# Kernel optimization log

Measured on AMD Instinct MI355X. Metric: run time of the kernel, lower is better.

The kernel has to match this reference:

```python
import jax, jax.numpy as jnp
import numpy as np

D_MODEL = 2048
NUM_HEADS = 32
NUM_GROUPS = 8
D_K = D_MODEL // NUM_HEADS          # 64
HPG = NUM_HEADS // NUM_GROUPS       # heads per group = 4
B, S = 2, 2048


def setup_inputs() -> dict:
    key = jax.random.key(0)
    ks = jax.random.split(key, 9)
    w_scale = 0.02
    kv_dim = NUM_GROUPS * D_K
    return {
        "x":  jax.random.normal(ks[0], (B, S, D_MODEL), dtype=jnp.float32),
        "Wq": jax.random.normal(ks[1], (D_MODEL, D_MODEL), dtype=jnp.float32) * w_scale,
        "bq": jnp.zeros((D_MODEL,), dtype=jnp.float32),
        "Wk": jax.random.normal(ks[2], (D_MODEL, kv_dim), dtype=jnp.float32) * w_scale,
        "bk": jnp.zeros((kv_dim,), dtype=jnp.float32),
        "Wv": jax.random.normal(ks[3], (D_MODEL, kv_dim), dtype=jnp.float32) * w_scale,
        "bv": jnp.zeros((kv_dim,), dtype=jnp.float32),
        "Wo": jax.random.normal(ks[4], (D_MODEL, D_MODEL), dtype=jnp.float32) * w_scale,
        "bo": jnp.zeros((D_MODEL,), dtype=jnp.float32),
    }


def reference(x, Wq, bq, Wk, bk, Wv, bv, Wo, bo):
    b, s, _ = x.shape
    # projections (torch Linear math: x @ W^T + b, here weights stored as (in,out))
    Q = (x @ Wq + bq).reshape(b, s, NUM_HEADS, D_K).transpose(0, 2, 1, 3)   # [B,H,S,dk]
    Kg = (x @ Wk + bk).reshape(b, s, NUM_GROUPS, D_K).transpose(0, 2, 1, 3)  # [B,G,S,dk]
    Vg = (x @ Wv + bv).reshape(b, s, NUM_GROUPS, D_K).transpose(0, 2, 1, 3)
    # repeat_interleave K/V over head dim to full head count
    K = jnp.repeat(Kg, HPG, axis=1)  # [B,H,S,dk]
    V = jnp.repeat(Vg, HPG, axis=1)
    scores = jnp.einsum("bhqd,bhkd->bhqk", Q, K) / np.sqrt(D_K).astype(np.float32)
    attn = jax.nn.softmax(scores, axis=-1)
    out = jnp.einsum("bhqk,bhkd->bhqd", attn, V)               # [B,H,S,dk]
    out = out.transpose(0, 2, 1, 3).reshape(b, s, D_MODEL)
    out = out @ Wo + bo
    # module returns grouped K,V cache: K[:, ::HPG] == Kg
    return out, (Kg, Vg)
```

## Files before the change

### kernel.cpp

```cpp
#include <hip/hip_runtime.h>
#include <hip/hip_bf16.h>
#include <stdint.h>

#define S_LEN 2048
#define DM    2048
#define NH    32
#define NG    8
#define DK    64
#define BATCH 2
#define MROWS (BATCH*S_LEN)
#define NQKV  3072
#define SSCALE 0.18033688f

typedef __bf16 bf16x8 __attribute__((ext_vector_type(8)));
typedef short  s16x8  __attribute__((ext_vector_type(8)));
typedef float  f32x4  __attribute__((ext_vector_type(4)));
typedef unsigned int u32x4 __attribute__((ext_vector_type(4)));

__device__ __forceinline__ unsigned short f2b(float f) {
    unsigned int x = __float_as_uint(f);
    unsigned int r = (x + 0x7fffu + ((x >> 16) & 1u)) >> 16;
    return (unsigned short)r;
}
__device__ __forceinline__ bf16x8 ld8(const unsigned short* p) {
    return *(const bf16x8*)p;
}
__device__ __forceinline__ s16x8 cvt8(const float* p) {
    f32x4 a = *(const f32x4*)p;
    f32x4 b = *(const f32x4*)(p + 4);
    s16x8 o;
#pragma unroll
    for (int j = 0; j < 4; j++) { o[j] = (short)f2b(a[j]); o[4 + j] = (short)f2b(b[j]); }
    return o;
}
__device__ __forceinline__ void gl_lds(const unsigned short* g, unsigned short* l) {
    __builtin_amdgcn_global_load_lds(
        (const __attribute__((address_space(1))) unsigned int*)g,
        (__attribute__((address_space(3))) unsigned int*)l, 16, 0, 0);
}
__device__ __forceinline__ void wait_dma() {
    asm volatile("s_waitcnt vmcnt(0)" ::: "memory");
}

__global__ __launch_bounds__(256) void cvt_x(const float* __restrict__ in,
                                             unsigned short* __restrict__ out) {
    size_t id = (size_t)blockIdx.x * 256 + threadIdx.x;
    *(s16x8*)&out[id * 8] = cvt8(in + id * 8);
}

__global__ void transpose_cvt(const float* __restrict__ in,
                              unsigned short* __restrict__ out, int R, int C) {
    __shared__ float t[32][33];
    int c0 = blockIdx.x * 32, r0 = blockIdx.y * 32;
    int tx = threadIdx.x, ty = threadIdx.y;
#pragma unroll
    for (int i = 0; i < 4; i++)
        t[ty + i * 8][tx] = in[(size_t)(r0 + ty + i * 8) * C + c0 + tx];
    __syncthreads();
#pragma unroll
    for (int i = 0; i < 4; i++)
        out[(size_t)(c0 + ty + i * 8) * R + r0 + tx] = f2b(t[tx][ty + i * 8]);
}

__global__ void bias_concat(const float* __restrict__ bq, const float* __restrict__ bk,
                            const float* __restrict__ bv, float* __restrict__ o) {
    int i = blockIdx.x * 256 + threadIdx.x;
    if (i < 2048) o[i] = bq[i];
    else if (i < 2560) o[i] = bk[i - 2048];
    else if (i < 3072) o[i] = bv[i - 2560];
}

__global__ __launch_bounds__(256) void gemm_qkv(const unsigned short* __restrict__ A,
                                                const unsigned short* __restrict__ Bt,
                                                const float* __restrict__ bias,
                                                unsigned short* __restrict__ Qb,
                                                float* __restrict__ Kg, float* __restrict__ Vg,
                                                unsigned short* __restrict__ Kb,
                                                unsigned short* __restrict__ Vtb) {
    __shared__ alignas(16) unsigned short As[128 * 32];
    __shared__ alignas(16) unsigned short Bs[128 * 32];
    const int K = DM;
    const int tid = threadIdx.x;
    const int n0 = blockIdx.x * 128, m0 = blockIdx.y * 128;
    const int w = tid >> 6, lane = tid & 63;
    const int ln15 = lane & 15, quad = lane >> 4;
    const int wm = (w >> 1) * 64, wn = (w & 1) * 64;
    const int xq = (quad ^ (ln15 & 3)) * 8;
    f32x4 acc[4][4] = {};
    for (int k0 = 0; k0 < K; k0 += 32) {
        __syncthreads();
#pragma unroll
        for (int i = 0; i < 2; ++i) {
            int s = w * 128 + i * 64 + lane;
            int r = s >> 2, cb = (s & 3) ^ (r & 3);
            gl_lds(&A[(size_t)(m0 + r) * K + k0 + cb * 8], &As[(w * 128 + i * 64) * 8]);
            gl_lds(&Bt[(size_t)(n0 + r) * K + k0 + cb * 8], &Bs[(w * 128 + i * 64) * 8]);
        }
        wait_dma();
        __syncthreads();
        bf16x8 af[4], bfr[4];
#pragma unroll
        for (int mt = 0; mt < 4; mt++)
            af[mt] = ld8(&As[(wm + mt * 16 + ln15) * 32 + xq]);
#pragma unroll
        for (int nt = 0; nt < 4; nt++)
            bfr[nt] = ld8(&Bs[(wn + nt * 16 + ln15) * 32 + xq]);
#pragma unroll
        for (int mt = 0; mt < 4; mt++)
#pragma unroll
            for (int nt = 0; nt < 4; nt++)
                acc[mt][nt] = __builtin_amdgcn_mfma_f32_16x16x32_bf16(af[mt], bfr[nt], acc[mt][nt], 0, 0, 0);
    }
#pragma unroll
    for (int nt = 0; nt < 4; nt++) {
        int col = n0 + wn + nt * 16 + ln15;
        float bv = bias[col];
#pragma unroll
        for (int mt = 0; mt < 4; mt++) {
            int row0 = m0 + wm + mt * 16 + quad * 4;
#pragma unroll
            for (int r = 0; r < 4; r++) {
                float val = acc[mt][nt][r] + bv;
                int row = row0 + r;
                int b = row >> 11, s = row & 2047;
                if (col < 2048) {
                    Qb[(size_t)row * DM + col] = f2b(val * SSCALE);
                } else if (col < 2560) {
                    int gc = col - 2048, g = gc >> 6, d = gc & 63;
                    size_t idx = (((size_t)(b * NG + g) * S_LEN + s) << 6) + d;
                    Kg[idx] = val;
                    Kb[idx] = f2b(val);
                } else {
                    int gc = col - 2560, g = gc >> 6, d = gc & 63;
                    Vg[(((size_t)(b * NG + g) * S_LEN + s) << 6) + d] = val;
                    Vtb[((size_t)(b * NG + g) * DK + d) * S_LEN + s] = f2b(val);
                }
            }
        }
    }
}

__global__ __launch_bounds__(256) void gemm_o(const unsigned short* __restrict__ A,
                                              const unsigned short* __restrict__ Bt,
                                              const float* __restrict__ bias,
                                              float* __restrict__ C) {
    __shared__ alignas(16) unsigned short As[128 * 32];
    __shared__ alignas(16) unsigned short Bs[128 * 32];
    const int K = DM, N = DM;
    const int tid = threadIdx.x;
    const int n0 = blockIdx.x * 128, m0 = blockIdx.y * 128;
    const int w = tid >> 6, lane = tid & 63;
    const int ln15 = lane & 15, quad = lane >> 4;
    const int wm = (w >> 1) * 64, wn = (w & 1) * 64;
    const int xq = (quad ^ (ln15 & 3)) * 8;
    f32x4 acc[4][4] = {};
    for (int k0 = 0; k0 < K; k0 += 32) {
        __syncthreads();
#pragma unroll
        for (int i = 0; i < 2; ++i) {
            int s = w * 128 + i * 64 + lane;
            int r = s >> 2, cb = (s & 3) ^ (r & 3);
            gl_lds(&A[(size_t)(m0 + r) * K + k0 + cb * 8], &As[(w * 128 + i * 64) * 8]);
            gl_lds(&Bt[(size_t)(n0 + r) * K + k0 + cb * 8], &Bs[(w * 128 + i * 64) * 8]);
        }
        wait_dma();
        __syncthreads();
        bf16x8 af[4], bfr[4];
#pragma unroll
        for (int mt = 0; mt < 4; mt++)
            af[mt] = ld8(&As[(wm + mt * 16 + ln15) * 32 + xq]);
#pragma unroll
        for (int nt = 0; nt < 4; nt++)
            bfr[nt] = ld8(&Bs[(wn + nt * 16 + ln15) * 32 + xq]);
#pragma unroll
        for (int mt = 0; mt < 4; mt++)
#pragma unroll
            for (int nt = 0; nt < 4; nt++)
                acc[mt][nt] = __builtin_amdgcn_mfma_f32_16x16x32_bf16(af[mt], bfr[nt], acc[mt][nt], 0, 0, 0);
    }
#pragma unroll
    for (int nt = 0; nt < 4; nt++) {
        int col = n0 + wn + nt * 16 + ln15;
        float bv = bias[col];
#pragma unroll
        for (int mt = 0; mt < 4; mt++) {
            int row0 = m0 + wm + mt * 16 + quad * 4;
#pragma unroll
            for (int r = 0; r < 4; r++)
                C[(size_t)(row0 + r) * N + col] = acc[mt][nt][r] + bv;
        }
    }
}

#define MT 2
__global__ __launch_bounds__(256, 4) void attn_fwd(const unsigned short* __restrict__ Qb,
                                                   const unsigned short* __restrict__ Kb,
                                                   const unsigned short* __restrict__ Vtb,
                                                   unsigned short* __restrict__ AO) {
    __shared__ alignas(16) unsigned short Ks[2][64 * 64];
    __shared__ alignas(16) unsigned short Vt[2][64 * 64];
    const int b = blockIdx.z, h = blockIdx.y, q0 = blockIdx.x * (MT * 64);
    const int g = h >> 2;
    const int tid = threadIdx.x;
    const int w = tid >> 6, lane = tid & 63;
    const int ln15 = lane & 15, quad = lane >> 4;
    const int x7a = (quad ^ (ln15 & 7)) * 8;
    const int x7b = x7a ^ 32;

    bf16x8 aq[MT][2];
#pragma unroll
    for (int mt = 0; mt < MT; mt++) {
        const size_t qrow =
            ((size_t)(b * S_LEN + q0 + w * (MT * 16) + mt * 16 + ln15)) * DM + h * DK;
        aq[mt][0] = ld8(&Qb[qrow + quad * 8]);
        aq[mt][1] = ld8(&Qb[qrow + 32 + quad * 8]);
    }

    bf16x8 ones;
#pragma unroll
    for (int j = 0; j < 8; j++) ones[j] = (__bf16)1.0f;

    f32x4 o[MT][4] = {};
    f32x4 l_acc[MT] = {};
    const size_t kvb = ((size_t)(b * NG + g)) * S_LEN * DK;

#define STAGE(k0v, buf) do {                                                     \
    _Pragma("unroll")                                                            \
    for (int i = 0; i < 2; i++) {                                                \
        int s = w * 128 + i * 64 + lane;                                         \
        int r = s >> 3, cb = (s & 7) ^ (r & 7);                                  \
        gl_lds(&Kb[kvb + (size_t)((k0v) + r) * DK + cb * 8],                     \
               &Ks[buf][(w * 128 + i * 64) * 8]);                                \
        gl_lds(&Vtb[kvb + (size_t)r * S_LEN + (k0v) + cb * 8],                   \
               &Vt[buf][(w * 128 + i * 64) * 8]);                                \
    } } while (0)

    STAGE(0, 0);
    wait_dma();
    __syncthreads();
    int cur = 0;

    for (int k0 = 0; k0 < S_LEN; k0 += 64) {
        if (k0 + 64 < S_LEN) STAGE(k0 + 64, cur ^ 1);

        f32x4 z[MT][4];
        __builtin_amdgcn_s_setprio(1);
#pragma unroll
        for (int nt = 0; nt < 4; nt++) {
            bf16x8 bk0 = ld8(&Ks[cur][(nt * 16 + ln15) * 64 + x7a]);
            bf16x8 bk1 = ld8(&Ks[cur][(nt * 16 + ln15) * 64 + x7b]);
#pragma unroll
            for (int mt = 0; mt < MT; mt++) {
                f32x4 t = {0.f, 0.f, 0.f, 0.f};
                t = __builtin_amdgcn_mfma_f32_16x16x32_bf16(bk0, aq[mt][0], t, 0, 0, 0);
                t = __builtin_amdgcn_mfma_f32_16x16x32_bf16(bk1, aq[mt][1], t, 0, 0, 0);
                z[mt][nt] = t;
            }
        }
        __builtin_amdgcn_s_setprio(0);

        bf16x8 pa[MT][2];
#pragma unroll
        for (int mt = 0; mt < MT; mt++) {
            unsigned int S[4][2];
#pragma unroll
            for (int nt = 0; nt < 4; nt++) {
                f32x4 pe;
#pragma unroll
                for (int r = 0; r < 4; r++)
                    pe[r] = __builtin_amdgcn_exp2f(z[mt][nt][r]);
                asm("v_cvt_pk_bf16_f32 %0, %1, %2" : "=v"(S[nt][0]) : "v"(pe[0]), "v"(pe[1]));
                asm("v_cvt_pk_bf16_f32 %0, %1, %2" : "=v"(S[nt][1]) : "v"(pe[2]), "v"(pe[3]));
            }
#pragma unroll
            for (int f = 0; f < 2; f++) {
                unsigned int wA[2], wB[2];
#pragma unroll
                for (int p = 0; p < 2; p++) {
                    unsigned int xa = S[2 * f][p], yb = S[2 * f + 1][p];
                    asm("v_permlane32_swap_b32 %0, %1" : "+v"(xa), "+v"(yb));
                    asm("v_permlane16_swap_b32 %0, %1" : "+v"(xa), "+v"(yb));
                    wA[p] = xa; wB[p] = yb;
                }
                u32x4 t4;
                t4[0] = wA[0]; t4[1] = wA[1]; t4[2] = wB[0]; t4[3] = wB[1];
                pa[mt][f] = __builtin_bit_cast(bf16x8, t4);
            }
        }

        __builtin_amdgcn_s_setprio(1);
#pragma unroll
        for (int nt = 0; nt < 4; nt++) {
            bf16x8 bv0 = ld8(&Vt[cur][(nt * 16 + ln15) * 64 + x7a]);
            bf16x8 bv1 = ld8(&Vt[cur][(nt * 16 + ln15) * 64 + x7b]);
#pragma unroll
            for (int mt = 0; mt < MT; mt++) {
                f32x4 t = o[mt][nt];
                t = __builtin_amdgcn_mfma_f32_16x16x32_bf16(pa[mt][0], bv0, t, 0, 0, 0);
                t = __builtin_amdgcn_mfma_f32_16x16x32_bf16(pa[mt][1], bv1, t, 0, 0, 0);
                o[mt][nt] = t;
            }
        }
#pragma unroll
        for (int mt = 0; mt < MT; mt++) {
            l_acc[mt] = __builtin_amdgcn_mfma_f32_16x16x32_bf16(pa[mt][0], ones, l_acc[mt], 0, 0, 0);
            l_acc[mt] = __builtin_amdgcn_mfma_f32_16x16x32_bf16(pa[mt][1], ones, l_acc[mt], 0, 0, 0);
        }
        __builtin_amdgcn_s_setprio(0);

        wait_dma();
        __syncthreads();
        cur ^= 1;
    }
#undef STAGE

#pragma unroll
    for (int mt = 0; mt < MT; mt++) {
#pragma unroll
        for (int r = 0; r < 4; r++) {
            float inv = 1.0f / l_acc[mt][r];
            int q = q0 + w * (MT * 16) + mt * 16 + quad * 4 + r;
#pragma unroll
            for (int nt = 0; nt < 4; nt++) {
                int col = h * DK + nt * 16 + ln15;
                *(__bf16*)&AO[((size_t)(b * S_LEN + q)) * DM + col] =
                    (__bf16)(o[mt][nt][r] * inv);
            }
        }
    }
}

extern "C" void kernel_launch(void* const* d_in, const int* in_sizes, int n_in,
                              void* d_out, int out_size, void* d_ws, size_t ws_size,
                              hipStream_t stream) {
    const float* x  = (const float*)d_in[0];
    const float* Wq = (const float*)d_in[1];
    const float* bq = (const float*)d_in[2];
    const float* Wk = (const float*)d_in[3];
    const float* bk = (const float*)d_in[4];
    const float* Wv = (const float*)d_in[5];
    const float* bv = (const float*)d_in[6];
    const float* Wo = (const float*)d_in[7];
    const float* bo = (const float*)d_in[8];

    float* out = (float*)d_out;
    float* Kg  = out + (size_t)MROWS * DM;
    float* Vg  = Kg + (size_t)BATCH * NG * S_LEN * DK;

    unsigned short* Qb = (unsigned short*)d_out;

    unsigned short* ws    = (unsigned short*)d_ws;
    unsigned short* WqkvT = ws;
    unsigned short* WoT   = WqkvT + (size_t)NQKV * DM;
    unsigned short* Kb    = WoT + (size_t)DM * DM;
    unsigned short* Vtb   = Kb + (size_t)BATCH * NG * S_LEN * DK;
    unsigned short* AO    = Vtb + (size_t)BATCH * NG * S_LEN * DK;
    unsigned short* xb    = AO + (size_t)MROWS * DM;
    float*          bqkv  = (float*)(xb + (size_t)MROWS * DM);

    hipLaunchKernelGGL(cvt_x, dim3(MROWS * DM / 8 / 256), dim3(256), 0, stream, x, xb);

    dim3 tb(32, 8);
    hipLaunchKernelGGL(transpose_cvt, dim3(DM / 32, DM / 32), tb, 0, stream,
                       Wq, WqkvT, DM, DM);
    hipLaunchKernelGGL(transpose_cvt, dim3(512 / 32, DM / 32), tb, 0, stream,
                       Wk, WqkvT + (size_t)2048 * DM, DM, 512);
    hipLaunchKernelGGL(transpose_cvt, dim3(512 / 32, DM / 32), tb, 0, stream,
                       Wv, WqkvT + (size_t)2560 * DM, DM, 512);
    hipLaunchKernelGGL(transpose_cvt, dim3(DM / 32, DM / 32), tb, 0, stream,
                       Wo, WoT, DM, DM);
    hipLaunchKernelGGL(bias_concat, dim3(12), dim3(256), 0, stream, bq, bk, bv, bqkv);

    hipLaunchKernelGGL(gemm_qkv, dim3(NQKV / 128, MROWS / 128), dim3(256), 0, stream,
                       xb, WqkvT, bqkv, Qb, Kg, Vg, Kb, Vtb);

    hipLaunchKernelGGL(attn_fwd, dim3(S_LEN / (MT * 64), NH, BATCH), dim3(256), 0, stream,
                       Qb, Kb, Vtb, AO);

    hipLaunchKernelGGL(gemm_o, dim3(DM / 128, MROWS / 128), dim3(256), 0, stream,
                       AO, WoT, bo, out);
}
```

Before: 360.2 us.

## Double-buffer LDS in QKV and output GEMMs with new swizzle and MFMA priority

Both projection GEMMs now keep two LDS stages, so the global-to-LDS DMA for the next K tile is issued before the current tile's MFMAs. This removes one barrier per iteration and overlaps load latency with compute. The LDS XOR swizzle changes from (row&3) to ((row>>1)&3) to cut bank conflicts. The MFMA block is wrapped in s_setprio and launch bounds now request 4 blocks per CU. The cost is doubled LDS use per block (32KB) and more register pressure.

```diff
diff --git a/kernel.cpp b/kernel.cpp
--- a/kernel.cpp
+++ b/kernel.cpp
@@ -70,47 +70,60 @@
     else if (i < 3072) o[i] = bv[i - 2560];
 }
 
-__global__ __launch_bounds__(256) void gemm_qkv(const unsigned short* __restrict__ A,
+__global__ __launch_bounds__(256, 4) void gemm_qkv(const unsigned short* __restrict__ A,
                                                 const unsigned short* __restrict__ Bt,
                                                 const float* __restrict__ bias,
                                                 unsigned short* __restrict__ Qb,
                                                 float* __restrict__ Kg, float* __restrict__ Vg,
                                                 unsigned short* __restrict__ Kb,
                                                 unsigned short* __restrict__ Vtb) {
-    __shared__ alignas(16) unsigned short As[128 * 32];
-    __shared__ alignas(16) unsigned short Bs[128 * 32];
+    __shared__ alignas(16) unsigned short As[2][128 * 32];
+    __shared__ alignas(16) unsigned short Bs[2][128 * 32];
     const int K = DM;
     const int tid = threadIdx.x;
     const int n0 = blockIdx.x * 128, m0 = blockIdx.y * 128;
     const int w = tid >> 6, lane = tid & 63;
     const int ln15 = lane & 15, quad = lane >> 4;
     const int wm = (w >> 1) * 64, wn = (w & 1) * 64;
-    const int xq = (quad ^ (ln15 & 3)) * 8;
+    const int xq = (quad ^ ((ln15 >> 1) & 3)) * 8;
     f32x4 acc[4][4] = {};
+
+#define GSTAGE(k0v, buf) do {                                                    \
+    _Pragma("unroll")                                                            \
+    for (int i = 0; i < 2; ++i) {                                                \
+        int s = w * 128 + i * 64 + lane;             \
+        int r = s >> 2, cb = (s & 3) ^ ((r >> 1) & 3);                           \
+        gl_lds(&A[(size_t)(m0 + r) * K + (k0v) + cb * 8],                        \
+               &As[buf][(w * 128 + i * 64) * 8]);                                \
+        gl_lds(&Bt[(size_t)(n0 + r) * K + (k0v) + cb * 8],                       \
+               &Bs[buf][(w * 128 + i * 64) * 8]);                                \
+    } } while (0)
+
+    GSTAGE(0, 0);
+    wait_dma();
+    __syncthreads();
+    int cur = 0;
     for (int k0 = 0; k0 < K; k0 += 32) {
-        __syncthreads();
-#pragma unroll
-        for (int i = 0; i < 2; ++i) {
-            int s = w * 128 + i * 64 + lane;
-            int r = s >> 2, cb = (s & 3) ^ (r & 3);
-            gl_lds(&A[(size_t)(m0 + r) * K + k0 + cb * 8], &As[(w * 128 + i * 64) * 8]);
-            gl_lds(&Bt[(size_t)(n0 + r) * K + k0 + cb * 8], &Bs[(w * 128 + i * 64) * 8]);
-        }
+        if (k0 + 32 < K) GSTAGE(k0 + 32, cur ^ 1);
+        bf16x8 af[4], bfr[4];
+#pragma unroll
+        for (int mt = 0; mt < 4; mt++)
+            af[mt] = ld8(&As[cur][(wm + mt * 16 + ln15) * 32 + xq]);
+#pragma unroll
+        for (int nt = 0; nt < 4; nt++)
+            bfr[nt] = ld8(&Bs[cur][(wn + nt * 16 + ln15) * 32 + xq]);
+        __builtin_amdgcn_s_setprio(1);
+#pragma unroll
+        for (int mt = 0; mt < 4; mt++)
+#pragma unroll
+            for (int nt = 0; nt < 4; nt++)
+                acc[mt][nt] = __builtin_amdgcn_mfma_f32_16x16x32_bf16(af[mt], bfr[nt], acc[mt][nt], 0, 0, 0);
+        __builtin_amdgcn_s_setprio(0);
         wait_dma();
         __syncthreads();
-        bf16x8 af[4], bfr[4];
-#pragma unroll
-        for (int mt = 0; mt < 4; mt++)
-            af[mt] = ld8(&As[(wm + mt * 16 + ln15) * 32 + xq]);
-#pragma unroll
-        for (int nt = 0; nt < 4; nt++)
-            bfr[nt] = ld8(&Bs[(wn + nt * 16 + ln15) * 32 + xq]);
-#pragma unroll
-        for (int mt = 0; mt < 4; mt++)
-#pragma unroll
-            for (int nt = 0; nt < 4; nt++)
-                acc[mt][nt] = __builtin_amdgcn_mfma_f32_16x16x32_bf16(af[mt], bfr[nt], acc[mt][nt], 0, 0, 0);
-    }
+        cur ^= 1;
+    }
+#undef GSTAGE
 #pragma unroll
     for (int nt = 0; nt < 4; nt++) {
         int col = n0 + wn + nt * 16 + ln15;
@@ -140,44 +153,57 @@
     }
 }
 
-__global__ __launch_bounds__(256) void gemm_o(const unsigned short* __restrict__ A,
+__global__ __launch_bounds__(256, 4) void gemm_o(const unsigned short* __restrict__ A,
                                               const unsigned short* __restrict__ Bt,
                                               const float* __restrict__ bias,
                                               float* __restrict__ C) {
-    __shared__ alignas(16) unsigned short As[128 * 32];
-    __shared__ alignas(16) unsigned short Bs[128 * 32];
+    __shared__ alignas(16) unsigned short As[2][128 * 32];
+    __shared__ alignas(16) unsigned short Bs[2][128 * 32];
     const int K = DM, N = DM;
     const int tid = threadIdx.x;
     const int n0 = blockIdx.x * 128, m0 = blockIdx.y * 128;
     const int w = tid >> 6, lane = tid & 63;
     const int ln15 = lane & 15, quad = lane >> 4;
     const int wm = (w >> 1) * 64, wn = (w & 1) * 64;
-    const int xq = (quad ^ (ln15 & 3)) * 8;
+    const int xq = (quad ^ ((ln15 >> 1) & 3)) * 8;
     f32x4 acc[4][4] = {};
+
+#define GSTAGE(k0v, buf) do {                                                    \
+    _Pragma("unroll")                                                            \
+    for (int i = 0; i < 2; ++i) {                                                \
+        int s = w * 128 + i * 64 + lane;                                         \
+        int r = s >> 2, cb = (s & 3) ^ ((r >> 1) & 3);                           \
+        gl_lds(&A[(size_t)(m0 + r) * K + (k0v) + cb * 8],                        \
+               &As[buf][(w * 128 + i * 64) * 8]);                                \
+        gl_lds(&Bt[(size_t)(n0 + r) * K + (k0v) + cb * 8],                       \
+               &Bs[buf][(w * 128 + i * 64) * 8]);                                \
+    } } while (0)
+
+    GSTAGE(0, 0);
+    wait_dma();
+    __syncthreads();
+    int cur = 0;
     for (int k0 = 0; k0 < K; k0 += 32) {
-        __syncthreads();
-#pragma unroll
-        for (int i = 0; i < 2; ++i) {
-            int s = w * 128 + i * 64 + lane;
-            int r = s >> 2, cb = (s & 3) ^ (r & 3);
-            gl_lds(&A[(size_t)(m0 + r) * K + k0 + cb * 8], &As[(w * 128 + i * 64) * 8]);
-            gl_lds(&Bt[(size_t)(n0 + r) * K + k0 + cb * 8], &Bs[(w * 128 + i * 64) * 8]);
-        }
+        if (k0 + 32 < K) GSTAGE(k0 + 32, cur ^ 1);
+        bf16x8 af[4], bfr[4];
+#pragma unroll
+        for (int mt = 0; mt < 4; mt++)
+            af[mt] = ld8(&As[cur][(wm + mt * 16 + ln15) * 32 + xq]);
+#pragma unroll
+        for (int nt = 0; nt < 4; nt++)
+            bfr[nt] = ld8(&Bs[cur][(wn + nt * 16 + ln15) * 32 + xq]);
+        __builtin_amdgcn_s_setprio(1);
+#pragma unroll
+        for (int mt = 0; mt < 4; mt++)
+#pragma unroll
+            for (int nt = 0; nt < 4; nt++)
+                acc[mt][nt] = __builtin_amdgcn_mfma_f32_16x16x32_bf16(af[mt], bfr[nt], acc[mt][nt], 0, 0, 0);
+        __builtin_amdgcn_s_setprio(0);
         wait_dma();
         __syncthreads();
-        bf16x8 af[4], bfr[4];
-#pragma unroll
-        for (int mt = 0; mt < 4; mt++)
-            af[mt] = ld8(&As[(wm + mt * 16 + ln15) * 32 + xq]);
-#pragma unroll
-        for (int nt = 0; nt < 4; nt++)
-            bfr[nt] = ld8(&Bs[(wn + nt * 16 + ln15) * 32 + xq]);
-#pragma unroll
-        for (int mt = 0; mt < 4; mt++)
-#pragma unroll
-            for (int nt = 0; nt < 4; nt++)
-                acc[mt][nt] = __builtin_amdgcn_mfma_f32_16x16x32_bf16(af[mt], bfr[nt], acc[mt][nt], 0, 0, 0);
-    }
+        cur ^= 1;
+    }
+#undef GSTAGE
 #pragma unroll
     for (int nt = 0; nt < 4; nt++) {
         int col = n0 + wn + nt * 16 + ln15;
```

After: 326.9 us. 1.1x faster.
